# Optimization experiments

Measured on AMD Instinct MI355X. Metric: run time of the kernel, lower is better.

Reference implementation:

```python
import jax, jax.numpy as jnp
import numpy as np

B, C_IN, L = 8, 64, 4096
C_OUT, HEADS = 64, 3
E = 524288
T_DIM = 256
N = B * L
EPS = 1e-5
NEG_SLOPE = 0.2  # PyG GATConv default negative_slope


def setup_inputs() -> dict:
    key = jax.random.key(0)
    ks = jax.random.split(key, 12)
    x = jax.random.normal(ks[0], (B, C_IN, L), jnp.float32)
    time_emb = jax.random.normal(ks[1], (B, T_DIM), jnp.float32)
    edge_index = jax.random.randint(ks[2], (2, E), 0, N, dtype=jnp.int32)
    # GATConv params: lin maps in -> heads*out; att_src/att_dst per head
    W_lin = jax.random.normal(ks[3], (C_IN, HEADS * C_OUT), jnp.float32) / np.sqrt(C_IN)
    att_src = jax.random.normal(ks[4], (1, HEADS, C_OUT), jnp.float32) / np.sqrt(C_OUT)
    att_dst = jax.random.normal(ks[5], (1, HEADS, C_OUT), jnp.float32) / np.sqrt(C_OUT)
    bias = jnp.zeros((C_OUT,), jnp.float32)
    # time projection (computed but unused in the source forward)
    tp_W = jax.random.normal(ks[6], (T_DIM, C_OUT), jnp.float32) / np.sqrt(T_DIM)
    tp_b = jnp.zeros((C_OUT,), jnp.float32)
    # BatchNorm1d affine params (training-mode batch stats)
    gamma = jnp.ones((C_OUT,), jnp.float32)
    beta = jnp.zeros((C_OUT,), jnp.float32)
    return {"x": x, "time_emb": time_emb, "edge_index": edge_index,
            "W_lin": W_lin, "att_src": att_src, "att_dst": att_dst,
            "bias": bias, "tp_W": tp_W, "tp_b": tp_b,
            "gamma": gamma, "beta": beta}


def reference(x, time_emb, edge_index, W_lin, att_src, att_dst, bias, tp_W, tp_b, gamma, beta):
    b, c, l = x.shape
    n = b * l
    # time projection: present in source but its result is never used
    _t = (time_emb @ tp_W + tp_b)[:, :, None]  # [b, C_OUT, 1] (dead)
    h = (x.reshape(-1, c) @ W_lin).reshape(n, HEADS, C_OUT)  # [N,H,C]
    a_src = (h * att_src).sum(-1)  # [N,H]
    a_dst = (h * att_dst).sum(-1)  # [N,H]
    # add self loops (PyG default add_self_loops=True)
    loops = jnp.arange(n, dtype=edge_index.dtype)
    src = jnp.concatenate([edge_index[0], loops])
    dst = jnp.concatenate([edge_index[1], loops])
    e = a_src[src] + a_dst[dst]                        # [E+N, H]
    e = jnp.where(e > 0, e, NEG_SLOPE * e)             # LeakyReLU
    emax = jax.ops.segment_max(e, dst, num_segments=n)  # every node has a self loop
    ex = jnp.exp(e - emax[dst])
    denom = jax.ops.segment_sum(ex, dst, num_segments=n)
    alpha = ex / denom[dst]                            # segment softmax over dst
    msg = alpha[:, :, None] * h[src]                   # [E+N, H, C]
    out = jax.ops.segment_sum(msg, dst, num_segments=n)  # [N,H,C]
    out = out.mean(axis=1) + bias                      # concat=False -> head mean
    # BatchNorm1d (training mode: biased batch stats)
    mu = out.mean(axis=0)
    var = ((out - mu) ** 2).mean(axis=0)
    out = (out - mu) / jnp.sqrt(var + EPS) * gamma + beta
    out = jax.nn.relu(out)
    return out.reshape(b, -1, l)
```

## Files before the change

kernel.cpp:

```cpp
#include <hip/hip_runtime.h>

#define N_NODES 32768
#define E_EDGES 524288
#define HC 192
#define NEG_SLOPE 0.2f
#define BN_EPS 1e-5f
#define PAD 64

typedef _Float16 f16;
typedef __attribute__((ext_vector_type(8))) _Float16 v8h;
typedef __attribute__((ext_vector_type(4))) float    v4f;

#define SC_BLOCKS 1536
#define K1_BLOCKS 2048
#define K2_BLOCKS 2048
#define APPLY_BLOCKS 512
#define ZROW 200

__device__ __forceinline__ float lrelu(float v) { return v > 0.f ? v : NEG_SLOPE * v; }

__device__ __forceinline__ float wave_sum(float v) {
#pragma unroll
    for (int off = 32; off > 0; off >>= 1) v += __shfl_xor(v, off);
    return v;
}

__global__ __launch_bounds__(256, 8) void k_build(
        const int* __restrict__ esrc, const int* __restrict__ edst,
        int* __restrict__ cnt, unsigned short* __restrict__ csr_pad,
        const float* __restrict__ x, const float* __restrict__ W,
        const float* __restrict__ att_s, const float* __restrict__ att_d,
        f16* __restrict__ x16, float* __restrict__ a_src, float* __restrict__ a_dst,
        f16* __restrict__ Wp, float* __restrict__ gp1, float* __restrict__ gp2) {
    const int bid = blockIdx.x;
    if (bid < SC_BLOCKS) {
        int i = bid * 256 + threadIdx.x;
        int s0 = esrc[i], d0 = edst[i];
        int s1 = 0, d1 = 0;
        const bool two = (bid < 512);
        if (two) { s1 = esrc[i + 393216]; d1 = edst[i + 393216]; }
        int p0 = atomicAdd(&cnt[d0 << 4], 1);
        int p1 = two ? atomicAdd(&cnt[d1 << 4], 1) : 0;
        if (p0 < PAD) csr_pad[d0 * PAD + p0] = (unsigned short)s0;
        if (two && p1 < PAD) csr_pad[d1 * PAD + p1] = (unsigned short)s1;
        return;
    }
    const int gid = bid - SC_BLOCKS;
    __shared__ float us[3][64], ud[3][64];
    if (threadIdx.x < 192) {
        const int h = threadIdx.x >> 6, k = threadIdx.x & 63;
        const float* wr = W + k * HC + h * 64;
        const float* ap = att_s + h * 64;
        const float* dp = att_d + h * 64;
        float su = 0.f, du = 0.f;
#pragma unroll
        for (int ch = 0; ch < 64; ch++) {
            float w = wr[ch];
            su = fmaf(w, ap[ch], su);
            du = fmaf(w, dp[ch], du);
        }
        us[h][k] = su; ud[h][k] = du;
    }
    if (gid == 0) {
        float4 z4 = make_float4(0.f, 0.f, 0.f, 0.f);
#pragma unroll
        for (int i = 0; i < 4; i++) {
            ((float4*)gp1)[threadIdx.x * 4 + i] = z4;
            ((float4*)gp2)[threadIdx.x * 4 + i] = z4;
        }
        for (int idx = threadIdx.x; idx < 1536; idx += 256) {
            const int kfct = idx >> 6, ln = idx & 63;
            const int kf = kfct >> 2, ct = kfct & 3;
            const int qq = ln >> 4, nn = ln & 15;
#pragma unroll
            for (int j = 0; j < 8; j++) {
                int kp = kf * 32 + qq * 8 + j;
                int h = kp >> 6, kk = kp & 63;
                Wp[(size_t)idx * 8 + j] = (f16)W[kk * HC + h * 64 + ct * 16 + nn];
            }
        }
    }
    __syncthreads();
    const int lane = threadIdx.x & 63, wv = threadIdx.x >> 6;
    const float u0 = us[0][lane], u1 = us[1][lane], u2 = us[2][lane];
    const float d0 = ud[0][lane], d1 = ud[1][lane], d2 = ud[2][lane];
    const int nbase = (gid * 4 + wv) * 16;
#pragma unroll 1
    for (int t = 0; t < 16; t++) {
        const int n = nbase + t;
        const float xv = x[n * 64 + lane];
        x16[n * 64 + lane] = (f16)xv;
        float s0 = wave_sum(xv * u0), s1 = wave_sum(xv * u1), s2 = wave_sum(xv * u2);
        float t0 = wave_sum(xv * d0), t1 = wave_sum(xv * d1), t2 = wave_sum(xv * d2);
        if (lane == 0) {
            ((float4*)a_src)[n] = make_float4(s0, s1, s2, 0.f);
            ((float4*)a_dst)[n] = make_float4(t0, t1, t2, 0.f);
        }
    }
}

__global__ __launch_bounds__(256, 8) void k_agg(
        const f16* __restrict__ x16,
        const float* __restrict__ a_src,
        const float* __restrict__ a_dst,
        const int* __restrict__ cnt,
        const unsigned short* __restrict__ csr_pad,
        const f16* __restrict__ Wp,
        const float* __restrict__ bias,
        float* __restrict__ out_pre,
        float* __restrict__ gp1, float* __restrict__ gp2) {
    const int lane = threadIdx.x & 63;
    const int wv = threadIdx.x >> 6;
    const int bid = blockIdx.x;
    const int n0 = bid * 16;

    __shared__ f16 zlds[16][ZROW];
    __shared__ float4 wsl[4][64];

#pragma unroll 1
    for (int r = 0; r < 4; r++) {
        const int n = n0 + (r << 2) + wv;
        int deg = cnt[n << 4]; if (deg > PAD) deg = PAD;
        const unsigned short* __restrict__ row = csr_pad + n * PAD;
        const float ad0 = a_dst[n * 4 + 0], ad1 = a_dst[n * 4 + 1], ad2 = a_dst[n * 4 + 2];
        float ws0 = __expf(lrelu(a_src[n * 4 + 0] + ad0));
        float ws1 = __expf(lrelu(a_src[n * 4 + 1] + ad1));
        float ws2 = __expf(lrelu(a_src[n * 4 + 2] + ad2));
        int s = 0;
        float w0 = 0.f, w1 = 0.f, w2 = 0.f;
        if (lane < deg) {
            s = (int)row[lane];
            float4 as = ((const float4*)a_src)[s];
            w0 = __expf(lrelu(as.x + ad0));
            w1 = __expf(lrelu(as.y + ad1));
            w2 = __expf(lrelu(as.z + ad2));
        }
        float den0 = ws0 + wave_sum(w0);
        float den1 = ws1 + wave_sum(w1);
        float den2 = ws2 + wave_sum(w2);
        const float i0 = 1.f / (3.f * den0);
        const float i1 = 1.f / (3.f * den1);
        const float i2 = 1.f / (3.f * den2);
        wsl[wv][lane] = make_float4(w0 * i0, w1 * i1, w2 * i2, 0.f);
        const float xs = (float)x16[(size_t)n * 64 + lane];
        float z0 = ws0 * i0 * xs, z1 = ws1 * i1 * xs, z2 = ws2 * i2 * xs;
        int j = 0;
        for (; j + 8 <= deg; j += 8) {
            int sj[8]; float xv[8];
#pragma unroll
            for (int u = 0; u < 8; u++) sj[u] = __builtin_amdgcn_readlane(s, j + u);
#pragma unroll
            for (int u = 0; u < 8; u++) xv[u] = (float)x16[(size_t)sj[u] * 64 + lane];
#pragma unroll
            for (int u = 0; u < 8; u++) {
                float4 wj = wsl[wv][j + u];
                z0 = fmaf(wj.x, xv[u], z0);
                z1 = fmaf(wj.y, xv[u], z1);
                z2 = fmaf(wj.z, xv[u], z2);
            }
        }
        for (; j < deg; j++) {
            int sa = __builtin_amdgcn_readlane(s, j);
            float xa = (float)x16[(size_t)sa * 64 + lane];
            float4 wj = wsl[wv][j];
            z0 = fmaf(wj.x, xa, z0);
            z1 = fmaf(wj.y, xa, z1);
            z2 = fmaf(wj.z, xa, z2);
        }
        const int rl = (r << 2) + wv;
        zlds[rl][lane]       = (f16)z0;
        zlds[rl][64 + lane]  = (f16)z1;
        zlds[rl][128 + lane] = (f16)z2;
    }
    __syncthreads();

    const int q = lane >> 4, nl = lane & 15;
    v4f C = {0.f, 0.f, 0.f, 0.f};
#pragma unroll
    for (int kf = 0; kf < 6; kf++) {
        v8h zb = *(const v8h*)(&zlds[nl][kf * 32 + q * 8]);
        v8h wa = *(const v8h*)(Wp + ((size_t)(kf * 4 + wv) * 64 + lane) * 8);
        C = __builtin_amdgcn_mfma_f32_16x16x32_f16(wa, zb, C, 0, 0, 0);
    }
    const int ch0 = wv * 16 + q * 4;
    float4 bv = *(const float4*)(bias + ch0);
    float o0 = C[0] + bv.x, o1 = C[1] + bv.y, o2 = C[2] + bv.z, o3 = C[3] + bv.w;
    *(float4*)(out_pre + (size_t)(n0 + nl) * 64 + ch0) = make_float4(o0, o1, o2, o3);
    float r0 = o0, r1 = o1, r2 = o2, r3 = o3;
    float q0 = o0 * o0, q1 = o1 * o1, q2 = o2 * o2, q3 = o3 * o3;
#pragma unroll
    for (int off = 1; off < 16; off <<= 1) {
        r0 += __shfl_xor(r0, off); r1 += __shfl_xor(r1, off);
        r2 += __shfl_xor(r2, off); r3 += __shfl_xor(r3, off);
        q0 += __shfl_xor(q0, off); q1 += __shfl_xor(q1, off);
        q2 += __shfl_xor(q2, off); q3 += __shfl_xor(q3, off);
    }
    if (nl == 0) {
        const int slice = bid & 63;
        float* g1 = gp1 + slice * 64 + ch0;
        float* g2 = gp2 + slice * 64 + ch0;
        atomicAdd(&g1[0], r0); atomicAdd(&g1[1], r1);
        atomicAdd(&g1[2], r2); atomicAdd(&g1[3], r3);
        atomicAdd(&g2[0], q0); atomicAdd(&g2[1], q1);
        atomicAdd(&g2[2], q2); atomicAdd(&g2[3], q3);
    }
}

__global__ __launch_bounds__(256) void k_apply(const float4* __restrict__ out_pre4,
                                               const float* __restrict__ gp1,
                                               const float* __restrict__ gp2,
                                               const float* __restrict__ gamma,
                                               const float* __restrict__ beta,
                                               float4* __restrict__ out4) {
    __shared__ float sc[64], sh[64];
    __shared__ float rs[256], rq[256];
    {
        const int t = threadIdx.x & 63, g = threadIdx.x >> 6;
        float s = 0.f, q = 0.f;
#pragma unroll
        for (int i = 0; i < 16; i++) {
            s += gp1[(g * 16 + i) * 64 + t];
            q += gp2[(g * 16 + i) * 64 + t];
        }
        rs[threadIdx.x] = s;
        rq[threadIdx.x] = q;
    }
    __syncthreads();
    if (threadIdx.x < 64) {
        int t = threadIdx.x;
        float s = rs[t] + rs[64 + t] + rs[128 + t] + rs[192 + t];
        float q = rq[t] + rq[64 + t] + rq[128 + t] + rq[192 + t];
        const float inv_n = 1.0f / (float)N_NODES;
        float mu = s * inv_n;
        float var = q * inv_n - mu * mu;
        float invstd = 1.0f / sqrtf(var + BN_EPS);
        float scale = invstd * gamma[t];
        sc[t] = scale;
        sh[t] = beta[t] - mu * scale;
    }
    __syncthreads();
    const int total = N_NODES * 64 / 4;
    for (int idx = blockIdx.x * 256 + threadIdx.x; idx < total; idx += APPLY_BLOCKS * 256) {
        int c0 = (idx * 4) & 63;
        float4 v = out_pre4[idx];
        float4 r;
        r.x = fmaxf(v.x * sc[c0 + 0] + sh[c0 + 0], 0.f);
        r.y = fmaxf(v.y * sc[c0 + 1] + sh[c0 + 1], 0.f);
        r.z = fmaxf(v.z * sc[c0 + 2] + sh[c0 + 2], 0.f);
        r.w = fmaxf(v.w * sc[c0 + 3] + sh[c0 + 3], 0.f);
        out4[idx] = r;
    }
}

extern "C" void kernel_launch(void* const* d_in, const int* in_sizes, int n_in,
                              void* d_out, int out_size, void* d_ws, size_t ws_size,
                              hipStream_t stream) {
    const float* x     = (const float*)d_in[0];
    const int*   ei    = (const int*)d_in[2];
    const float* W     = (const float*)d_in[3];
    const float* att_s = (const float*)d_in[4];
    const float* att_d = (const float*)d_in[5];
    const float* bias  = (const float*)d_in[6];
    const float* gamma = (const float*)d_in[9];
    const float* beta  = (const float*)d_in[10];
    float* out = (float*)d_out;

    char* ws = (char*)d_ws;
    size_t off = 0;
    auto alloc = [&](size_t bytes) -> void* {
        void* p = ws + off;
        off += (bytes + 255) & ~(size_t)255;
        return p;
    };
    int*            cnt     = (int*)alloc((size_t)N_NODES * 16 * 4);
    unsigned short* csr_pad = (unsigned short*)alloc((size_t)N_NODES * PAD * 2);
    f16*            x16     = (f16*)alloc((size_t)N_NODES * 64 * 2);
    float*          a_src   = (float*)alloc((size_t)N_NODES * 4 * 4);
    float*          a_dst   = (float*)alloc((size_t)N_NODES * 4 * 4);
    f16*            Wp      = (f16*)alloc((size_t)1536 * 8 * 2);
    float*          gp1     = (float*)alloc(64 * 64 * 4);
    float*          gp2     = (float*)alloc(64 * 64 * 4);
    float*          out_pre = (float*)alloc((size_t)N_NODES * 64 * 4);

    hipMemsetAsync(cnt, 0, (size_t)N_NODES * 16 * 4, stream);

    k_build<<<K1_BLOCKS, 256, 0, stream>>>(
        ei, ei + E_EDGES, cnt, csr_pad,
        x, W, att_s, att_d, x16, a_src, a_dst, Wp, gp1, gp2);
    k_agg<<<K2_BLOCKS, 256, 0, stream>>>(x16, a_src, a_dst, cnt, csr_pad, Wp,
                                         bias, out_pre, gp1, gp2);
    k_apply<<<APPLY_BLOCKS, 256, 0, stream>>>((const float4*)out_pre, gp1, gp2,
                                              gamma, beta, (float4*)out);
}
```

Measured before the change: 161.6 us.

## Replace global-atomic CSR build with chunked LDS histogram, scan, and scatter

Measured after the change: 167.3 us. +3.5%, slower.

```diff
diff --git a/kernel.cpp b/kernel.cpp
--- a/kernel.cpp
+++ b/kernel.cpp
@@ -11,9 +11,16 @@
 typedef __attribute__((ext_vector_type(8))) _Float16 v8h;
 typedef __attribute__((ext_vector_type(4))) float    v4f;
 
-#define SC_BLOCKS 1536
-#define K1_BLOCKS 2048
-#define K2_BLOCKS 2048
+#define NCHUNK 128
+#define CHK_E  4096
+#define NRANGE 4
+#define RNG_N  8192
+
+#define HIST_BLOCKS (NCHUNK * NRANGE)
+#define K1_BLOCKS   (HIST_BLOCKS + 512)
+#define K2_BLOCKS   (N_NODES / 256)
+#define K3_BLOCKS   HIST_BLOCKS
+#define K4_BLOCKS   (N_NODES / 16)
 #define APPLY_BLOCKS 512
 #define ZROW 200
 
@@ -25,28 +32,31 @@
     return v;
 }
 
-__global__ __launch_bounds__(256, 8) void k_build(
+__global__ __launch_bounds__(256, 4) void k_build(
         const int* __restrict__ esrc, const int* __restrict__ edst,
-        int* __restrict__ cnt, unsigned short* __restrict__ csr_pad,
+        int* __restrict__ H,
         const float* __restrict__ x, const float* __restrict__ W,
         const float* __restrict__ att_s, const float* __restrict__ att_d,
         f16* __restrict__ x16, float* __restrict__ a_src, float* __restrict__ a_dst,
         f16* __restrict__ Wp, float* __restrict__ gp1, float* __restrict__ gp2) {
     const int bid = blockIdx.x;
-    if (bid < SC_BLOCKS) {
-        int i = bid * 256 + threadIdx.x;
-        int s0 = esrc[i], d0 = edst[i];
-        int s1 = 0, d1 = 0;
-        const bool two = (bid < 512);
-        if (two) { s1 = esrc[i + 393216]; d1 = edst[i + 393216]; }
-        int p0 = atomicAdd(&cnt[d0 << 4], 1);
-        int p1 = two ? atomicAdd(&cnt[d1 << 4], 1) : 0;
-        if (p0 < PAD) csr_pad[d0 * PAD + p0] = (unsigned short)s0;
-        if (two && p1 < PAD) csr_pad[d1 * PAD + p1] = (unsigned short)s1;
+    __shared__ int hist[RNG_N];
+    __shared__ float us[3][64], ud[3][64];
+    if (bid < HIST_BLOCKS) {
+        const int c = bid >> 2, r = bid & 3;
+        for (int i = threadIdx.x; i < RNG_N; i += 256) hist[i] = 0;
+        __syncthreads();
+        const int* __restrict__ dp = edst + c * CHK_E;
+        for (int i = threadIdx.x; i < CHK_E; i += 256) {
+            int d = dp[i];
+            if ((d >> 13) == r) atomicAdd(&hist[d & (RNG_N - 1)], 1);
+        }
+        __syncthreads();
+        int* __restrict__ Hrow = H + (size_t)c * N_NODES + r * RNG_N;
+        for (int i = threadIdx.x; i < RNG_N; i += 256) Hrow[i] = hist[i];
         return;
     }
-    const int gid = bid - SC_BLOCKS;
-    __shared__ float us[3][64], ud[3][64];
+    const int gid = bid - HIST_BLOCKS;
     if (threadIdx.x < 192) {
         const int h = threadIdx.x >> 6, k = threadIdx.x & 63;
         const float* wr = W + k * HC + h * 64;
@@ -99,6 +109,40 @@
     }
 }
 
+__global__ __launch_bounds__(256) void k_scan(int* __restrict__ H,
+                                              int* __restrict__ cnt) {
+    const int n = blockIdx.x * 256 + threadIdx.x;
+    int run = 0;
+#pragma unroll 4
+    for (int c = 0; c < NCHUNK; c++) {
+        int v = H[(size_t)c * N_NODES + n];
+        H[(size_t)c * N_NODES + n] = run;
+        run += v;
+    }
+    cnt[n] = run;
+}
+
+__global__ __launch_bounds__(256, 4) void k_scatter(
+        const int* __restrict__ esrc, const int* __restrict__ edst,
+        const int* __restrict__ H, unsigned short* __restrict__ csr_pad) {
+    const int c = blockIdx.x >> 2, r = blockIdx.x & 3;
+    __shared__ int hist[RNG_N];
+    for (int i = threadIdx.x; i < RNG_N; i += 256) hist[i] = 0;
+    __syncthreads();
+    const int* __restrict__ dp = edst + c * CHK_E;
+    const int* __restrict__ sp = esrc + c * CHK_E;
+    const int* __restrict__ Ho = H + (size_t)c * N_NODES;
+    for (int i = threadIdx.x; i < CHK_E; i += 256) {
+        int d = dp[i];
+        if ((d >> 13) == r) {
+            int lr = atomicAdd(&hist[d & (RNG_N - 1)], 1);
+            int slot = Ho[d] + lr;
+            int s = sp[i];
+            if (slot < PAD) csr_pad[d * PAD + slot] = (unsigned short)s;
+        }
+    }
+}
+
 __global__ __launch_bounds__(256, 8) void k_agg(
         const f16* __restrict__ x16,
         const float* __restrict__ a_src,
@@ -120,7 +164,7 @@
 #pragma unroll 1
     for (int r = 0; r < 4; r++) {
         const int n = n0 + (r << 2) + wv;
-        int deg = cnt[n << 4]; if (deg > PAD) deg = PAD;
+        int deg = cnt[n]; if (deg > PAD) deg = PAD;
         const unsigned short* __restrict__ row = csr_pad + n * PAD;
         const float ad0 = a_dst[n * 4 + 0], ad1 = a_dst[n * 4 + 1], ad2 = a_dst[n * 4 + 2];
         float ws0 = __expf(lrelu(a_src[n * 4 + 0] + ad0));
@@ -272,7 +316,8 @@
         off += (bytes + 255) & ~(size_t)255;
         return p;
     };
-    int*            cnt     = (int*)alloc((size_t)N_NODES * 16 * 4);
+    int*            H       = (int*)alloc((size_t)NCHUNK * N_NODES * 4);
+    int*            cnt     = (int*)alloc((size_t)N_NODES * 4);
     unsigned short* csr_pad = (unsigned short*)alloc((size_t)N_NODES * PAD * 2);
     f16*            x16     = (f16*)alloc((size_t)N_NODES * 64 * 2);
     float*          a_src   = (float*)alloc((size_t)N_NODES * 4 * 4);
@@ -282,12 +327,14 @@
     float*          gp2     = (float*)alloc(64 * 64 * 4);
     float*          out_pre = (float*)alloc((size_t)N_NODES * 64 * 4);
 
-    hipMemsetAsync(cnt, 0, (size_t)N_NODES * 16 * 4, stream);
+    const int* esrc = ei;
+    const int* edst = ei + E_EDGES;
 
     k_build<<<K1_BLOCKS, 256, 0, stream>>>(
-        ei, ei + E_EDGES, cnt, csr_pad,
-        x, W, att_s, att_d, x16, a_src, a_dst, Wp, gp1, gp2);
-    k_agg<<<K2_BLOCKS, 256, 0, stream>>>(x16, a_src, a_dst, cnt, csr_pad, Wp,
+        esrc, edst, H, x, W, att_s, att_d, x16, a_src, a_dst, Wp, gp1, gp2);
+    k_scan<<<K2_BLOCKS, 256, 0, stream>>>(H, cnt);
+    k_scatter<<<K3_BLOCKS, 256, 0, stream>>>(esrc, edst, H, csr_pad);
+    k_agg<<<K4_BLOCKS, 256, 0, stream>>>(x16, a_src, a_dst, cnt, csr_pad, Wp,
                                          bias, out_pre, gp1, gp2);
     k_apply<<<APPLY_BLOCKS, 256, 0, stream>>>((const float4*)out_pre, gp1, gp2,
                                               gamma, beta, (float4*)out);
```

## Build CSR with LDS histograms per chunk/range and drop global atomics

Applied to the files above, without the earlier changes.

After: 194.8 us. 1.21x slower.

```diff
diff --git a/kernel.cpp b/kernel.cpp
--- a/kernel.cpp
+++ b/kernel.cpp
@@ -5,18 +5,25 @@
 #define HC 192
 #define NEG_SLOPE 0.2f
 #define BN_EPS 1e-5f
-#define PAD 64
+
+#define NCHUNK 16
+#define CHK_E  32768
+#define CAP    12
+#define PAD    (NCHUNK * CAP)
+#define NRANGE 16
+#define RNG_N  2048
+
+#define SCT_BLOCKS (NCHUNK * NRANGE)
+#define K1_BLOCKS  (SCT_BLOCKS + 512)
+#define K2_BLOCKS  (N_NODES / 16)
+#define K3_BLOCKS  64
+#define APPLY_BLOCKS 512
+#define ZROW 200
 
 typedef _Float16 f16;
 typedef __attribute__((ext_vector_type(8))) _Float16 v8h;
 typedef __attribute__((ext_vector_type(4))) float    v4f;
 
-#define SC_BLOCKS 1536
-#define K1_BLOCKS 2048
-#define K2_BLOCKS 2048
-#define APPLY_BLOCKS 512
-#define ZROW 200
-
 __device__ __forceinline__ float lrelu(float v) { return v > 0.f ? v : NEG_SLOPE * v; }
 
 __device__ __forceinline__ float wave_sum(float v) {
@@ -27,26 +34,37 @@
 
 __global__ __launch_bounds__(256, 8) void k_build(
         const int* __restrict__ esrc, const int* __restrict__ edst,
-        int* __restrict__ cnt, unsigned short* __restrict__ csr_pad,
+        unsigned short* __restrict__ csr_pad,
+        unsigned short* __restrict__ cnt16,
         const float* __restrict__ x, const float* __restrict__ W,
         const float* __restrict__ att_s, const float* __restrict__ att_d,
         f16* __restrict__ x16, float* __restrict__ a_src, float* __restrict__ a_dst,
-        f16* __restrict__ Wp, float* __restrict__ gp1, float* __restrict__ gp2) {
+        f16* __restrict__ Wp) {
     const int bid = blockIdx.x;
-    if (bid < SC_BLOCKS) {
-        int i = bid * 256 + threadIdx.x;
-        int s0 = esrc[i], d0 = edst[i];
-        int s1 = 0, d1 = 0;
-        const bool two = (bid < 512);
-        if (two) { s1 = esrc[i + 393216]; d1 = edst[i + 393216]; }
-        int p0 = atomicAdd(&cnt[d0 << 4], 1);
-        int p1 = two ? atomicAdd(&cnt[d1 << 4], 1) : 0;
-        if (p0 < PAD) csr_pad[d0 * PAD + p0] = (unsigned short)s0;
-        if (two && p1 < PAD) csr_pad[d1 * PAD + p1] = (unsigned short)s1;
+    __shared__ int hist[RNG_N];
+    __shared__ float us[3][64], ud[3][64];
+    if (bid < SCT_BLOCKS) {
+        const int c = bid >> 4, r = bid & 15;
+        for (int i = threadIdx.x; i < RNG_N; i += 256) hist[i] = 0;
+        __syncthreads();
+        const int* __restrict__ dp = edst + c * CHK_E;
+        const int* __restrict__ sp = esrc + c * CHK_E;
+        for (int i = threadIdx.x; i < CHK_E; i += 256) {
+            int d = dp[i];
+            if ((d >> 11) == r) {
+                int lr = atomicAdd(&hist[d & (RNG_N - 1)], 1);
+                if (lr < CAP)
+                    csr_pad[(size_t)d * PAD + c * CAP + lr] = (unsigned short)sp[i];
+            }
+        }
+        __syncthreads();
+        for (int i = threadIdx.x; i < RNG_N; i += 256) {
+            int v = hist[i]; if (v > CAP) v = CAP;
+            cnt16[(size_t)(r * RNG_N + i) * NCHUNK + c] = (unsigned short)v;
+        }
         return;
     }
-    const int gid = bid - SC_BLOCKS;
-    __shared__ float us[3][64], ud[3][64];
+    const int gid = bid - SCT_BLOCKS;
     if (threadIdx.x < 192) {
         const int h = threadIdx.x >> 6, k = threadIdx.x & 63;
         const float* wr = W + k * HC + h * 64;
@@ -62,12 +80,6 @@
         us[h][k] = su; ud[h][k] = du;
     }
     if (gid == 0) {
-        float4 z4 = make_float4(0.f, 0.f, 0.f, 0.f);
-#pragma unroll
-        for (int i = 0; i < 4; i++) {
-            ((float4*)gp1)[threadIdx.x * 4 + i] = z4;
-            ((float4*)gp2)[threadIdx.x * 4 + i] = z4;
-        }
         for (int idx = threadIdx.x; idx < 1536; idx += 256) {
             const int kfct = idx >> 6, ln = idx & 63;
             const int kf = kfct >> 2, ct = kfct & 3;
@@ -103,12 +115,12 @@
         const f16* __restrict__ x16,
         const float* __restrict__ a_src,
         const float* __restrict__ a_dst,
-        const int* __restrict__ cnt,
+        const unsigned short* __restrict__ cnt16,
         const unsigned short* __restrict__ csr_pad,
         const f16* __restrict__ Wp,
         const float* __restrict__ bias,
         float* __restrict__ out_pre,
-        float* __restrict__ gp1, float* __restrict__ gp2) {
+        float* __restrict__ gps1, float* __restrict__ gps2) {
     const int lane = threadIdx.x & 63;
     const int wv = threadIdx.x >> 6;
     const int bid = blockIdx.x;
@@ -120,8 +132,19 @@
 #pragma unroll 1
     for (int r = 0; r < 4; r++) {
         const int n = n0 + (r << 2) + wv;
-        int deg = cnt[n << 4]; if (deg > PAD) deg = PAD;
-        const unsigned short* __restrict__ row = csr_pad + n * PAD;
+        const unsigned int* __restrict__ cp =
+            (const unsigned int*)(cnt16 + (size_t)n * NCHUNK);
+        int pfx = 0, myslot = 0;
+#pragma unroll
+        for (int u = 0; u < 8; u++) {
+            unsigned int w = cp[u];
+            int c0 = (int)(w & 0xffffu), c1 = (int)(w >> 16);
+            if (lane >= pfx && lane < pfx + c0) myslot = (2 * u) * CAP + (lane - pfx);
+            pfx += c0;
+            if (lane >= pfx && lane < pfx + c1) myslot = (2 * u + 1) * CAP + (lane - pfx);
+            pfx += c1;
+        }
+        int deg = pfx > 64 ? 64 : pfx;
         const float ad0 = a_dst[n * 4 + 0], ad1 = a_dst[n * 4 + 1], ad2 = a_dst[n * 4 + 2];
         float ws0 = __expf(lrelu(a_src[n * 4 + 0] + ad0));
         float ws1 = __expf(lrelu(a_src[n * 4 + 1] + ad1));
@@ -129,7 +152,7 @@
         int s = 0;
         float w0 = 0.f, w1 = 0.f, w2 = 0.f;
         if (lane < deg) {
-            s = (int)row[lane];
+            s = (int)csr_pad[(size_t)n * PAD + myslot];
             float4 as = ((const float4*)a_src)[s];
             w0 = __expf(lrelu(as.x + ad0));
             w1 = __expf(lrelu(as.y + ad1));
@@ -196,13 +219,34 @@
         q2 += __shfl_xor(q2, off); q3 += __shfl_xor(q3, off);
     }
     if (nl == 0) {
-        const int slice = bid & 63;
-        float* g1 = gp1 + slice * 64 + ch0;
-        float* g2 = gp2 + slice * 64 + ch0;
-        atomicAdd(&g1[0], r0); atomicAdd(&g1[1], r1);
-        atomicAdd(&g1[2], r2); atomicAdd(&g1[3], r3);
-        atomicAdd(&g2[0], q0); atomicAdd(&g2[1], q1);
-        atomicAdd(&g2[2], q2); atomicAdd(&g2[3], q3);
+        float* g1 = gps1 + (size_t)bid * 64 + ch0;
+        float* g2 = gps2 + (size_t)bid * 64 + ch0;
+        g1[0] = r0; g1[1] = r1; g1[2] = r2; g1[3] = r3;
+        g2[0] = q0; g2[1] = q1; g2[2] = q2; g2[3] = q3;
+    }
+}
+
+__global__ __launch_bounds__(256) void k_red(const float* __restrict__ gps1,
+                                             const float* __restrict__ gps2,
+                                             float* __restrict__ gp1,
+                                             float* __restrict__ gp2) {
+    const int b = blockIdx.x;
+    const int ch = threadIdx.x & 63, g = threadIdx.x >> 6;
+    __shared__ float r1[4][64], r2[4][64];
+    float s1 = 0.f, s2 = 0.f;
+#pragma unroll
+    for (int rr = 0; rr < 8; rr++) {
+        int row = b * 32 + g * 8 + rr;
+        s1 += gps1[row * 64 + ch];
+        s2 += gps2[row * 64 + ch];
+    }
+    r1[g][ch] = s1; r2[g][ch] = s2;
+    __syncthreads();
+    if (threadIdx.x < 64) {
+        gp1[b * 64 + threadIdx.x] = r1[0][threadIdx.x] + r1[1][threadIdx.x]
+                                  + r1[2][threadIdx.x] + r1[3][threadIdx.x];
+        gp2[b * 64 + threadIdx.x] = r2[0][threadIdx.x] + r2[1][threadIdx.x]
+                                  + r2[2][threadIdx.x] + r2[3][threadIdx.x];
     }
 }
 
@@ -272,23 +316,26 @@
         off += (bytes + 255) & ~(size_t)255;
         return p;
     };
-    int*            cnt     = (int*)alloc((size_t)N_NODES * 16 * 4);
     unsigned short* csr_pad = (unsigned short*)alloc((size_t)N_NODES * PAD * 2);
+    unsigned short* cnt16   = (unsigned short*)alloc((size_t)N_NODES * NCHUNK * 2);
     f16*            x16     = (f16*)alloc((size_t)N_NODES * 64 * 2);
     float*          a_src   = (float*)alloc((size_t)N_NODES * 4 * 4);
     float*          a_dst   = (float*)alloc((size_t)N_NODES * 4 * 4);
     f16*            Wp      = (f16*)alloc((size_t)1536 * 8 * 2);
+    float*          gps1    = (float*)alloc((size_t)K2_BLOCKS * 64 * 4);
+    float*          gps2    = (float*)alloc((size_t)K2_BLOCKS * 64 * 4);
     float*          gp1     = (float*)alloc(64 * 64 * 4);
     float*          gp2     = (float*)alloc(64 * 64 * 4);
     float*          out_pre = (float*)alloc((size_t)N_NODES * 64 * 4);
 
-    hipMemsetAsync(cnt, 0, (size_t)N_NODES * 16 * 4, stream);
+    const int* esrc = ei;
+    const int* edst = ei + E_EDGES;
 
     k_build<<<K1_BLOCKS, 256, 0, stream>>>(
-        ei, ei + E_EDGES, cnt, csr_pad,
-        x, W, att_s, att_d, x16, a_src, a_dst, Wp, gp1, gp2);
-    k_agg<<<K2_BLOCKS, 256, 0, stream>>>(x16, a_src, a_dst, cnt, csr_pad, Wp,
-                                         bias, out_pre, gp1, gp2);
+        esrc, edst, csr_pad, cnt16, x, W, att_s, att_d, x16, a_src, a_dst, Wp);
+    k_agg<<<K2_BLOCKS, 256, 0, stream>>>(x16, a_src, a_dst, cnt16, csr_pad, Wp,
+                                         bias, out_pre, gps1, gps2);
+    k_red<<<K3_BLOCKS, 256, 0, stream>>>(gps1, gps2, gp1, gp2);
     k_apply<<<APPLY_BLOCKS, 256, 0, stream>>>((const float4*)out_pre, gp1, gp2,
                                               gamma, beta, (float4*)out);
 }
```
